# Optimization experiments

Hardware: AMD Instinct MI355X
Metric: run time of the kernel (lower is better)

## Reference

```python
import jax, jax.numpy as jnp
import numpy as np

N = 100000
F_IN = 512
NHID = 16
HEADS = 8
NCLASS = 40
E = 1600000
NEG_SLOPE = 0.2


def gat_conv(x, W, att_src, att_dst, bias, src, dst, heads, out_ch, concat):
    n = x.shape[0]
    h = (x @ W).reshape(n, heads, out_ch)              # [N,H,C]
    a_src = jnp.sum(h * att_src, axis=-1)              # [N,H]
    a_dst = jnp.sum(h * att_dst, axis=-1)              # [N,H]
    e = a_src[src] + a_dst[dst]                        # [E,H]
    e = jnp.where(e > 0, e, NEG_SLOPE * e)             # leaky_relu
    # segment softmax over incoming edges per destination node
    m = jax.ops.segment_max(e, dst, num_segments=n)    # [N,H]
    m = jnp.where(jnp.isfinite(m), m, 0.0)
    ex = jnp.exp(e - m[dst])
    s = jax.ops.segment_sum(ex, dst, num_segments=n)   # [N,H]
    alpha = ex / s[dst]                                # [E,H] (self-loops guarantee s>0)
    out = jax.ops.segment_sum(h[src] * alpha[:, :, None], dst, num_segments=n)  # [N,H,C]
    if concat:
        out = out.reshape(n, heads * out_ch)
    else:
        out = out.mean(axis=1)
    return out + bias


def setup_inputs() -> dict:
    key = jax.random.key(0)
    ks = jax.random.split(key, 10)
    x = jax.random.normal(ks[0], (N, F_IN), dtype=jnp.float32)
    edge_index = jax.random.randint(ks[1], (2, E), 0, N, dtype=jnp.int64)
    g1 = 1.0 / np.sqrt(F_IN)
    g2 = 1.0 / np.sqrt(NHID * HEADS)
    W1 = jax.random.uniform(ks[2], (F_IN, HEADS * NHID), jnp.float32, -g1, g1)
    att_src1 = jax.random.normal(ks[3], (1, HEADS, NHID), dtype=jnp.float32) * 0.1
    att_dst1 = jax.random.normal(ks[4], (1, HEADS, NHID), dtype=jnp.float32) * 0.1
    b1 = jnp.zeros((HEADS * NHID,), dtype=jnp.float32)
    W2 = jax.random.uniform(ks[5], (HEADS * NHID, NCLASS), jnp.float32, -g2, g2)
    att_src2 = jax.random.normal(ks[6], (1, 1, NCLASS), dtype=jnp.float32) * 0.1
    att_dst2 = jax.random.normal(ks[7], (1, 1, NCLASS), dtype=jnp.float32) * 0.1
    b2 = jnp.zeros((NCLASS,), dtype=jnp.float32)
    return {"x": x, "edge_index": edge_index, "W1": W1, "att_src1": att_src1,
            "att_dst1": att_dst1, "b1": b1, "W2": W2, "att_src2": att_src2,
            "att_dst2": att_dst2, "b2": b2}


def reference(x, edge_index, W1, att_src1, att_dst1, b1, W2, att_src2, att_dst2, b2):
    n = x.shape[0]
    # add self-loops (PyG GATConv default)
    loops = jnp.arange(n, dtype=edge_index.dtype)
    src = jnp.concatenate([edge_index[0], loops])
    dst = jnp.concatenate([edge_index[1], loops])
    # dropout is identity in eval mode
    h = gat_conv(x, W1, att_src1, att_dst1, b1, src, dst, HEADS, NHID, True)
    h = jax.nn.elu(h)
    out = gat_conv(h, W2, att_src2, att_dst2, b2, src, dst, 1, NCLASS, False)
    return jax.nn.log_softmax(out, axis=1)
```

## Files before the change

kernel.cpp:

```cpp
#include <hip/hip_runtime.h>
#include <hip/hip_fp16.h>
#include <math.h>

#define NEG_SLOPE 0.2f

__global__ __launch_bounds__(256) void gemm1_kernel(
    const float* __restrict__ x, const float* __restrict__ W,
    const float* __restrict__ att_src, const float* __restrict__ att_dst,
    __half* __restrict__ h1, float* __restrict__ a_src, float* __restrict__ a_dst,
    int M)
{
  __shared__ float At[32][68];
  __shared__ float Bs[32][128];
  const int tid = threadIdx.x;
  const int row0 = blockIdx.x * 64;
  const int tcol = (tid & 31) * 4;
  const int trow = (tid >> 5) * 8;
  float acc[8][4];
  #pragma unroll
  for (int i = 0; i < 8; i++)
    #pragma unroll
    for (int j = 0; j < 4; j++) acc[i][j] = 0.f;

  for (int k0 = 0; k0 < 512; k0 += 32) {
    #pragma unroll
    for (int i = 0; i < 2; ++i) {
      int idx = tid + i * 256;
      int r = idx >> 3;
      int kc = (idx & 7) << 2;
      float4 v = make_float4(0.f, 0.f, 0.f, 0.f);
      if (row0 + r < M) v = *(const float4*)&x[(size_t)(row0 + r) * 512 + k0 + kc];
      At[kc + 0][r] = v.x; At[kc + 1][r] = v.y; At[kc + 2][r] = v.z; At[kc + 3][r] = v.w;
    }
    #pragma unroll
    for (int i = 0; i < 4; ++i) {
      int idx = tid + i * 256;
      int kk = idx >> 5;
      int cc = (idx & 31) << 2;
      *(float4*)&Bs[kk][cc] = *(const float4*)&W[(size_t)(k0 + kk) * 128 + cc];
    }
    __syncthreads();
    #pragma unroll
    for (int k = 0; k < 32; ++k) {
      float4 b = *(float4*)&Bs[k][tcol];
      float4 a0 = *(float4*)&At[k][trow];
      float4 a1 = *(float4*)&At[k][trow + 4];
      float av[8] = {a0.x, a0.y, a0.z, a0.w, a1.x, a1.y, a1.z, a1.w};
      float bv[4] = {b.x, b.y, b.z, b.w};
      #pragma unroll
      for (int i = 0; i < 8; i++)
        #pragma unroll
        for (int j = 0; j < 4; j++)
          acc[i][j] = fmaf(av[i], bv[j], acc[i][j]);
    }
    __syncthreads();
  }
  float as1[4], ad1[4];
  #pragma unroll
  for (int j = 0; j < 4; j++) { as1[j] = att_src[tcol + j]; ad1[j] = att_dst[tcol + j]; }
  const int head = tcol >> 4;
  #pragma unroll
  for (int i = 0; i < 8; i++) {
    int r = row0 + trow + i;
    float ps = acc[i][0]*as1[0] + acc[i][1]*as1[1] + acc[i][2]*as1[2] + acc[i][3]*as1[3];
    float pd = acc[i][0]*ad1[0] + acc[i][1]*ad1[1] + acc[i][2]*ad1[2] + acc[i][3]*ad1[3];
    ps += __shfl_xor(ps, 1); ps += __shfl_xor(ps, 2);
    pd += __shfl_xor(pd, 1); pd += __shfl_xor(pd, 2);
    if (r < M) {
      __half2 p0 = __floats2half2_rn(acc[i][0], acc[i][1]);
      __half2 p1 = __floats2half2_rn(acc[i][2], acc[i][3]);
      uint2 u = make_uint2(*(unsigned int*)&p0, *(unsigned int*)&p1);
      *(uint2*)&h1[(size_t)r * 128 + tcol] = u;
      if ((tid & 3) == 0) { a_src[r * 8 + head] = ps; a_dst[r * 8 + head] = pd; }
    }
  }
}

__global__ __launch_bounds__(256) void hist_kernel(
    const int* __restrict__ ei, int E, int ET, int* __restrict__ cnt)
{
  int e = blockIdx.x * 256 + threadIdx.x;
  if (e >= ET) return;
  int dst = (e < E) ? ei[E + e] : e - E;
  atomicAdd(&cnt[dst], 1);
}

__global__ __launch_bounds__(256) void scan_bsum(
    const int* __restrict__ cnt, int* __restrict__ bsum, int M)
{
  __shared__ int sm[256];
  int i = blockIdx.x * 256 + threadIdx.x;
  sm[threadIdx.x] = (i < M) ? cnt[i] : 0;
  __syncthreads();
  for (int o = 128; o; o >>= 1) {
    if (threadIdx.x < o) sm[threadIdx.x] += sm[threadIdx.x + o];
    __syncthreads();
  }
  if (threadIdx.x == 0) bsum[blockIdx.x] = sm[0];
}

__global__ __launch_bounds__(512) void scan_boff(
    const int* __restrict__ bsum, int* __restrict__ boff, int NB)
{
  __shared__ int sm[512];
  int t = threadIdx.x;
  int v = (t < NB) ? bsum[t] : 0;
  sm[t] = v; __syncthreads();
  #pragma unroll
  for (int o = 1; o < 512; o <<= 1) {
    int add = (t >= o) ? sm[t - o] : 0;
    __syncthreads();
    sm[t] += add;
    __syncthreads();
  }
  boff[t] = sm[t] - v;
}

__global__ __launch_bounds__(256) void scan_final(
    const int* __restrict__ cnt, const int* __restrict__ boff,
    int* __restrict__ startp, int* __restrict__ cursor, int M)
{
  __shared__ int sm[256];
  int t = threadIdx.x;
  int i = blockIdx.x * 256 + t;
  int v = (i < M) ? cnt[i] : 0;
  sm[t] = v; __syncthreads();
  #pragma unroll
  for (int o = 1; o < 256; o <<= 1) {
    int add = (t >= o) ? sm[t - o] : 0;
    __syncthreads();
    sm[t] += add;
    __syncthreads();
  }
  int excl = sm[t] - v + boff[blockIdx.x];
  if (i < M) {
    startp[i] = excl;
    cursor[i] = excl;
    if (i == M - 1) startp[M] = excl + v;
  }
}

__global__ __launch_bounds__(256) void scatter_kernel(
    const int* __restrict__ ei, int E, int ET,
    int* __restrict__ cursor, int* __restrict__ ssrc)
{
  int e = blockIdx.x * 256 + threadIdx.x;
  if (e >= ET) return;
  int src, dst;
  if (e < E) { src = ei[e]; dst = ei[E + e]; }
  else { src = e - E; dst = src; }
  int pos = atomicAdd(&cursor[dst], 1);
  ssrc[pos] = src;
}

__global__ __launch_bounds__(256) void agg1_kernel(
    const int* __restrict__ startp, const int* __restrict__ ssrc,
    const float* __restrict__ a_s, const float* __restrict__ a_d,
    const __half* __restrict__ h1, const float* __restrict__ b1,
    __half* __restrict__ h1e, int M)
{
  int n = blockIdx.x * 4 + (threadIdx.x >> 6);
  if (n >= M) return;
  const int lane = threadIdx.x & 63;
  const int hd = lane >> 3;
  const __half2* hp = (const __half2*)h1;
  float ad = a_d[n * 8 + hd];
  int jb = startp[n], je = startp[n + 1];
  float acc0 = 0.f, acc1 = 0.f, ssum = 0.f;
  int j = jb;
  for (; j + 3 < je; j += 4) {
    int s0 = ssrc[j], s1 = ssrc[j+1], s2 = ssrc[j+2], s3 = ssrc[j+3];
    float e0 = a_s[s0 * 8 + hd] + ad;
    float e1 = a_s[s1 * 8 + hd] + ad;
    float e2 = a_s[s2 * 8 + hd] + ad;
    float e3 = a_s[s3 * 8 + hd] + ad;
    __half2 g0 = hp[(size_t)s0 * 64 + lane];
    __half2 g1 = hp[(size_t)s1 * 64 + lane];
    __half2 g2 = hp[(size_t)s2 * 64 + lane];
    __half2 g3 = hp[(size_t)s3 * 64 + lane];
    e0 = e0 > 0.f ? e0 : NEG_SLOPE * e0;
    e1 = e1 > 0.f ? e1 : NEG_SLOPE * e1;
    e2 = e2 > 0.f ? e2 : NEG_SLOPE * e2;
    e3 = e3 > 0.f ? e3 : NEG_SLOPE * e3;
    float x0 = __expf(e0), x1 = __expf(e1), x2 = __expf(e2), x3 = __expf(e3);
    float2 f0 = __half22float2(g0), f1 = __half22float2(g1);
    float2 f2 = __half22float2(g2), f3 = __half22float2(g3);
    acc0 = fmaf(x0, f0.x, acc0); acc1 = fmaf(x0, f0.y, acc1);
    acc0 = fmaf(x1, f1.x, acc0); acc1 = fmaf(x1, f1.y, acc1);
    acc0 = fmaf(x2, f2.x, acc0); acc1 = fmaf(x2, f2.y, acc1);
    acc0 = fmaf(x3, f3.x, acc0); acc1 = fmaf(x3, f3.y, acc1);
    ssum += (x0 + x1) + (x2 + x3);
  }
  for (; j < je; ++j) {
    int s0 = ssrc[j];
    float e0 = a_s[s0 * 8 + hd] + ad;
    e0 = e0 > 0.f ? e0 : NEG_SLOPE * e0;
    float x0 = __expf(e0);
    float2 f0 = __half22float2(hp[(size_t)s0 * 64 + lane]);
    acc0 = fmaf(x0, f0.x, acc0); acc1 = fmaf(x0, f0.y, acc1);
    ssum += x0;
  }
  float2 bv = *(const float2*)&b1[lane * 2];
  float v0 = acc0 / ssum + bv.x;
  float v1 = acc1 / ssum + bv.y;
  v0 = v0 > 0.f ? v0 : expm1f(v0);
  v1 = v1 > 0.f ? v1 : expm1f(v1);
  ((__half2*)h1e)[(size_t)n * 64 + lane] = __floats2half2_rn(v0, v1);
}

__global__ __launch_bounds__(256) void gemm2_kernel(
    const __half* __restrict__ h, const float* __restrict__ W2,
    const float* __restrict__ att_src, const float* __restrict__ att_dst,
    __half* __restrict__ h2, float* __restrict__ a2s, float* __restrict__ a2d,
    int M)
{
  __shared__ float W2s[128 * 40];
  __shared__ float hs[4][128];
  const int tid = threadIdx.x;
  const int lane = tid & 63;
  const int w = tid >> 6;
  const __half2* hp = (const __half2*)h;
  for (int i = tid; i < 128 * 40; i += 256) W2s[i] = W2[i];
  float asv = (lane < 40) ? att_src[lane] : 0.f;
  float adv = (lane < 40) ? att_dst[lane] : 0.f;
  __syncthreads();
  for (int r0 = blockIdx.x * 4; r0 < M; r0 += gridDim.x * 4) {
    {
      int r = r0 + (tid >> 6);
      int cp = tid & 63;
      float2 f = make_float2(0.f, 0.f);
      if (r < M) f = __half22float2(hp[(size_t)r * 64 + cp]);
      hs[tid >> 6][cp * 2] = f.x; hs[tid >> 6][cp * 2 + 1] = f.y;
    }
    __syncthreads();
    const int row = r0 + w;
    float acc = 0.f;
    if (lane < 40) {
      #pragma unroll 8
      for (int k = 0; k < 128; ++k) acc = fmaf(hs[w][k], W2s[k * 40 + lane], acc);
    }
    float ps = acc * asv, pd = acc * adv;
    #pragma unroll
    for (int off = 32; off; off >>= 1) { ps += __shfl_xor(ps, off); pd += __shfl_xor(pd, off); }
    if (row < M) {
      if (lane < 40) h2[(size_t)row * 40 + lane] = __float2half_rn(acc);
      if (lane == 0) { a2s[row] = ps; a2d[row] = pd; }
    }
    __syncthreads();
  }
}

__global__ __launch_bounds__(256) void agg2_kernel(
    const int* __restrict__ startp, const int* __restrict__ ssrc,
    const float* __restrict__ a2s, const float* __restrict__ a2d,
    const __half* __restrict__ h2, const float* __restrict__ b2,
    float* __restrict__ outp, int M)
{
  int n = blockIdx.x * 8 + (threadIdx.x >> 5);
  if (n >= M) return;
  const int l = threadIdx.x & 31;
  const bool act = l < 20;
  const __half2* hp = (const __half2*)h2;
  float ad = a2d[n];
  int jb = startp[n], je = startp[n + 1];
  float acc0 = 0.f, acc1 = 0.f, ssum = 0.f;
  __half2 z2 = __floats2half2_rn(0.f, 0.f);
  int j = jb;
  for (; j + 3 < je; j += 4) {
    int s0 = ssrc[j], s1 = ssrc[j+1], s2 = ssrc[j+2], s3 = ssrc[j+3];
    float e0 = a2s[s0] + ad;
    float e1 = a2s[s1] + ad;
    float e2 = a2s[s2] + ad;
    float e3 = a2s[s3] + ad;
    __half2 g0 = act ? hp[(size_t)s0 * 20 + l] : z2;
    __half2 g1 = act ? hp[(size_t)s1 * 20 + l] : z2;
    __half2 g2 = act ? hp[(size_t)s2 * 20 + l] : z2;
    __half2 g3 = act ? hp[(size_t)s3 * 20 + l] : z2;
    e0 = e0 > 0.f ? e0 : NEG_SLOPE * e0;
    e1 = e1 > 0.f ? e1 : NEG_SLOPE * e1;
    e2 = e2 > 0.f ? e2 : NEG_SLOPE * e2;
    e3 = e3 > 0.f ? e3 : NEG_SLOPE * e3;
    float x0 = __expf(e0), x1 = __expf(e1), x2 = __expf(e2), x3 = __expf(e3);
    float2 f0 = __half22float2(g0), f1 = __half22float2(g1);
    float2 f2 = __half22float2(g2), f3 = __half22float2(g3);
    acc0 = fmaf(x0, f0.x, acc0); acc1 = fmaf(x0, f0.y, acc1);
    acc0 = fmaf(x1, f1.x, acc0); acc1 = fmaf(x1, f1.y, acc1);
    acc0 = fmaf(x2, f2.x, acc0); acc1 = fmaf(x2, f2.y, acc1);
    acc0 = fmaf(x3, f3.x, acc0); acc1 = fmaf(x3, f3.y, acc1);
    ssum += (x0 + x1) + (x2 + x3);
  }
  for (; j < je; ++j) {
    int s0 = ssrc[j];
    float e0 = a2s[s0] + ad;
    e0 = e0 > 0.f ? e0 : NEG_SLOPE * e0;
    float x0 = __expf(e0);
    float2 f0 = __half22float2(act ? hp[(size_t)s0 * 20 + l] : z2);
    acc0 = fmaf(x0, f0.x, acc0); acc1 = fmaf(x0, f0.y, acc1);
    ssum += x0;
  }
  float v0 = act ? acc0 / ssum + b2[l * 2]     : -1e30f;
  float v1 = act ? acc1 / ssum + b2[l * 2 + 1] : -1e30f;
  float m = fmaxf(v0, v1);
  #pragma unroll
  for (int o = 16; o; o >>= 1) m = fmaxf(m, __shfl_xor(m, o));
  float ex = act ? expf(v0 - m) + expf(v1 - m) : 0.f;
  #pragma unroll
  for (int o = 16; o; o >>= 1) ex += __shfl_xor(ex, o);
  float lg = m + logf(ex);
  if (act) *(float2*)&outp[(size_t)n * 40 + l * 2] = make_float2(v0 - lg, v1 - lg);
}

extern "C" void kernel_launch(void* const* d_in, const int* in_sizes, int n_in,
                              void* d_out, int out_size, void* d_ws, size_t ws_size,
                              hipStream_t stream)
{
  const float* x   = (const float*)d_in[0];
  const int*   ei  = (const int*)d_in[1];
  const float* W1  = (const float*)d_in[2];
  const float* as1 = (const float*)d_in[3];
  const float* ad1 = (const float*)d_in[4];
  const float* b1  = (const float*)d_in[5];
  const float* W2  = (const float*)d_in[6];
  const float* as2 = (const float*)d_in[7];
  const float* ad2 = (const float*)d_in[8];
  const float* b2  = (const float*)d_in[9];
  float* outp = (float*)d_out;

  const int M  = in_sizes[0] / 512;
  const int E  = in_sizes[1] / 2;
  const int ET = E + M;
  const int NB = (M + 255) / 256;

  __half* h1  = (__half*)d_ws;
  __half* h1e = h1 + (size_t)M * 128;
  __half* h2  = h1e + (size_t)M * 128;
  float* a_s1 = (float*)(h2 + (size_t)M * 40);
  float* a_d1 = a_s1 + (size_t)M * 8;
  float* a2s  = a_d1 + (size_t)M * 8;
  float* a2d  = a2s + M;
  int* cnt    = (int*)(a2d + M);
  int* startp = cnt + M;
  int* cursor = startp + (M + 1);
  int* bsum   = cursor + M;
  int* boff   = bsum + NB;
  int* ssrc   = boff + 512;

  hipMemsetAsync(cnt, 0, (size_t)M * sizeof(int), stream);

  hist_kernel<<<(ET + 255) / 256, 256, 0, stream>>>(ei, E, ET, cnt);
  scan_bsum<<<NB, 256, 0, stream>>>(cnt, bsum, M);
  scan_boff<<<1, 512, 0, stream>>>(bsum, boff, NB);
  scan_final<<<NB, 256, 0, stream>>>(cnt, boff, startp, cursor, M);
  scatter_kernel<<<(ET + 255) / 256, 256, 0, stream>>>(ei, E, ET, cursor, ssrc);

  gemm1_kernel<<<(M + 63) / 64, 256, 0, stream>>>(x, W1, as1, ad1, h1, a_s1, a_d1, M);
  agg1_kernel<<<(M + 3) / 4, 256, 0, stream>>>(startp, ssrc, a_s1, a_d1, h1, b1, h1e, M);

  gemm2_kernel<<<1024, 256, 0, stream>>>(h1e, W2, as2, ad2, h2, a2s, a2d, M);
  agg2_kernel<<<(M + 7) / 8, 256, 0, stream>>>(startp, ssrc, a2s, a2d, h2, b2, outp, M);
}
```

Baseline: 843.4 us.

## Use bf16 MFMA for first-layer GEMM with swizzled LDS tiles

Replaces the scalar FP32 FMA tiled GEMM for x@W1 with a bf16 MFMA (16x16x32) kernel that uses 128-row tiles and XOR-swizzled shared memory. x is converted to bf16 on the fly, and a new small kernel pre-transposes and converts W1 to bf16. The attention dot products are now reduced with wave shuffles over the MFMA output layout. This cuts the compute cost of the dominant dense GEMM at the price of bf16 input rounding and narrower, scattered half stores in the epilogue.

```diff
diff --git a/kernel.cpp b/kernel.cpp
--- a/kernel.cpp
+++ b/kernel.cpp
@@ -4,74 +4,120 @@
 
 #define NEG_SLOPE 0.2f
 
+typedef short bf16x8 __attribute__((ext_vector_type(8)));
+typedef float f32x4 __attribute__((ext_vector_type(4)));
+
+__device__ __forceinline__ unsigned short f2bf(float f) {
+  unsigned int u = __builtin_bit_cast(unsigned int, f);
+  u = (u + 0x7fffu + ((u >> 16) & 1u)) >> 16;
+  return (unsigned short)u;
+}
+__device__ __forceinline__ unsigned int pk2bf(float lo, float hi) {
+  return (unsigned int)f2bf(lo) | ((unsigned int)f2bf(hi) << 16);
+}
+
+__global__ __launch_bounds__(256) void w1conv_kernel(
+    const float* __restrict__ W1, unsigned short* __restrict__ Wt)
+{
+  int idx = blockIdx.x * 256 + threadIdx.x;
+  int k = idx >> 7, n = idx & 127;
+  Wt[n * 512 + k] = f2bf(W1[idx]);
+}
+
 __global__ __launch_bounds__(256) void gemm1_kernel(
-    const float* __restrict__ x, const float* __restrict__ W,
+    const float* __restrict__ x, const unsigned short* __restrict__ Wt,
     const float* __restrict__ att_src, const float* __restrict__ att_dst,
     __half* __restrict__ h1, float* __restrict__ a_src, float* __restrict__ a_dst,
     int M)
 {
-  __shared__ float At[32][68];
-  __shared__ float Bs[32][128];
-  const int tid = threadIdx.x;
-  const int row0 = blockIdx.x * 64;
-  const int tcol = (tid & 31) * 4;
-  const int trow = (tid >> 5) * 8;
-  float acc[8][4];
-  #pragma unroll
-  for (int i = 0; i < 8; i++)
+  __shared__ unsigned char Asm[128 * 128];
+  __shared__ unsigned char Bsm[128 * 128];
+  const int tid  = threadIdx.x;
+  const int lane = tid & 63;
+  const int wid  = tid >> 6;
+  const int wr   = wid >> 1, wc = wid & 1;
+  const int row0 = blockIdx.x * 128;
+
+  f32x4 acc[4][4];
+  #pragma unroll
+  for (int m = 0; m < 4; ++m)
     #pragma unroll
-    for (int j = 0; j < 4; j++) acc[i][j] = 0.f;
-
-  for (int k0 = 0; k0 < 512; k0 += 32) {
+    for (int n = 0; n < 4; ++n) acc[m][n] = (f32x4){0.f, 0.f, 0.f, 0.f};
+
+  const int sr = tid >> 1;
+  const int sk = (tid & 1) * 32;
+  const int swz = (sr & 7) << 4;
+
+  for (int k0 = 0; k0 < 512; k0 += 64) {
+    {
+      const bool valid = (row0 + sr) < M;
+      const float4* src = (const float4*)&x[(size_t)(row0 + sr) * 512 + k0 + sk];
+      #pragma unroll
+      for (int q = 0; q < 4; ++q) {
+        float4 fa = valid ? src[q * 2]     : make_float4(0.f, 0.f, 0.f, 0.f);
+        float4 fb = valid ? src[q * 2 + 1] : make_float4(0.f, 0.f, 0.f, 0.f);
+        uint4 u = make_uint4(pk2bf(fa.x, fa.y), pk2bf(fa.z, fa.w),
+                             pk2bf(fb.x, fb.y), pk2bf(fb.z, fb.w));
+        *(uint4*)(Asm + sr * 128 + (((sk + q * 8) * 2) ^ swz)) = u;
+      }
+    }
+    {
+      const uint4* src = (const uint4*)&Wt[(size_t)sr * 512 + k0 + sk];
+      #pragma unroll
+      for (int q = 0; q < 4; ++q)
+        *(uint4*)(Bsm + sr * 128 + (((sk + q * 8) * 2) ^ swz)) = src[q];
+    }
+    __syncthreads();
     #pragma unroll
-    for (int i = 0; i < 2; ++i) {
-      int idx = tid + i * 256;
-      int r = idx >> 3;
-      int kc = (idx & 7) << 2;
-      float4 v = make_float4(0.f, 0.f, 0.f, 0.f);
-      if (row0 + r < M) v = *(const float4*)&x[(size_t)(row0 + r) * 512 + k0 + kc];
-      At[kc + 0][r] = v.x; At[kc + 1][r] = v.y; At[kc + 2][r] = v.z; At[kc + 3][r] = v.w;
-    }
+    for (int ks = 0; ks < 2; ++ks) {
+      const int kb = ks * 64 + ((lane >> 4) * 16);
+      bf16x8 af[4], bfr[4];
+      #pragma unroll
+      for (int m = 0; m < 4; ++m) {
+        int r = wr * 64 + m * 16 + (lane & 15);
+        af[m] = *(const bf16x8*)(Asm + r * 128 + (kb ^ ((r & 7) << 4)));
+      }
+      #pragma unroll
+      for (int n = 0; n < 4; ++n) {
+        int r = wc * 64 + n * 16 + (lane & 15);
+        bfr[n] = *(const bf16x8*)(Bsm + r * 128 + (kb ^ ((r & 7) << 4)));
+      }
+      #pragma unroll
+      for (int m = 0; m < 4; ++m)
+        #pragma unroll
+        for (int n = 0; n < 4; ++n)
+          acc[m][n] = __builtin_amdgcn_mfma_f32_16x16x32_bf16(af[m], bfr[n], acc[m][n], 0, 0, 0);
+    }
+    __syncthreads();
+  }
+
+  float asv[4], adv[4];
+  #pragma unroll
+  for (int n = 0; n < 4; ++n) {
+    int col = wc * 64 + n * 16 + (lane & 15);
+    asv[n] = att_src[col];
+    adv[n] = att_dst[col];
+  }
+  #pragma unroll
+  for (int m = 0; m < 4; ++m) {
     #pragma unroll
-    for (int i = 0; i < 4; ++i) {
-      int idx = tid + i * 256;
-      int kk = idx >> 5;
-      int cc = (idx & 31) << 2;
-      *(float4*)&Bs[kk][cc] = *(const float4*)&W[(size_t)(k0 + kk) * 128 + cc];
-    }
-    __syncthreads();
-    #pragma unroll
-    for (int k = 0; k < 32; ++k) {
-      float4 b = *(float4*)&Bs[k][tcol];
-      float4 a0 = *(float4*)&At[k][trow];
-      float4 a1 = *(float4*)&At[k][trow + 4];
-      float av[8] = {a0.x, a0.y, a0.z, a0.w, a1.x, a1.y, a1.z, a1.w};
-      float bv[4] = {b.x, b.y, b.z, b.w};
-      #pragma unroll
-      for (int i = 0; i < 8; i++)
-        #pragma unroll
-        for (int j = 0; j < 4; j++)
-          acc[i][j] = fmaf(av[i], bv[j], acc[i][j]);
-    }
-    __syncthreads();
-  }
-  float as1[4], ad1[4];
-  #pragma unroll
-  for (int j = 0; j < 4; j++) { as1[j] = att_src[tcol + j]; ad1[j] = att_dst[tcol + j]; }
-  const int head = tcol >> 4;
-  #pragma unroll
-  for (int i = 0; i < 8; i++) {
-    int r = row0 + trow + i;
-    float ps = acc[i][0]*as1[0] + acc[i][1]*as1[1] + acc[i][2]*as1[2] + acc[i][3]*as1[3];
-    float pd = acc[i][0]*ad1[0] + acc[i][1]*ad1[1] + acc[i][2]*ad1[2] + acc[i][3]*ad1[3];
-    ps += __shfl_xor(ps, 1); ps += __shfl_xor(ps, 2);
-    pd += __shfl_xor(pd, 1); pd += __shfl_xor(pd, 2);
-    if (r < M) {
-      __half2 p0 = __floats2half2_rn(acc[i][0], acc[i][1]);
-      __half2 p1 = __floats2half2_rn(acc[i][2], acc[i][3]);
-      uint2 u = make_uint2(*(unsigned int*)&p0, *(unsigned int*)&p1);
-      *(uint2*)&h1[(size_t)r * 128 + tcol] = u;
-      if ((tid & 3) == 0) { a_src[r * 8 + head] = ps; a_dst[r * 8 + head] = pd; }
+    for (int n = 0; n < 4; ++n) {
+      const int col  = wc * 64 + n * 16 + (lane & 15);
+      const int head = wc * 4 + n;
+      #pragma unroll
+      for (int e = 0; e < 4; ++e) {
+        int row = row0 + wr * 64 + m * 16 + (lane >> 4) * 4 + e;
+        float v = acc[m][n][e];
+        float ps = v * asv[n], pd = v * adv[n];
+        ps += __shfl_xor(ps, 1); pd += __shfl_xor(pd, 1);
+        ps += __shfl_xor(ps, 2); pd += __shfl_xor(pd, 2);
+        ps += __shfl_xor(ps, 4); pd += __shfl_xor(pd, 4);
+        ps += __shfl_xor(ps, 8); pd += __shfl_xor(pd, 8);
+        if (row < M) {
+          h1[(size_t)row * 128 + col] = __float2half_rn(v);
+          if ((lane & 15) == 0) { a_src[row * 8 + head] = ps; a_dst[row * 8 + head] = pd; }
+        }
+      }
     }
   }
 }
@@ -344,6 +390,7 @@
   int* bsum   = cursor + M;
   int* boff   = bsum + NB;
   int* ssrc   = boff + 512;
+  unsigned short* Wt = (unsigned short*)(ssrc + ET);
 
   hipMemsetAsync(cnt, 0, (size_t)M * sizeof(int), stream);
 
@@ -353,7 +400,8 @@
   scan_final<<<NB, 256, 0, stream>>>(cnt, boff, startp, cursor, M);
   scatter_kernel<<<(ET + 255) / 256, 256, 0, stream>>>(ei, E, ET, cursor, ssrc);
 
-  gemm1_kernel<<<(M + 63) / 64, 256, 0, stream>>>(x, W1, as1, ad1, h1, a_s1, a_d1, M);
+  w1conv_kernel<<<256, 256, 0, stream>>>(W1, Wt);
+  gemm1_kernel<<<(M + 127) / 128, 256, 0, stream>>>(x, Wt, as1, ad1, h1, a_s1, a_d1, M);
   agg1_kernel<<<(M + 3) / 4, 256, 0, stream>>>(startp, ssrc, a_s1, a_d1, h1, b1, h1e, M);
 
   gemm2_kernel<<<1024, 256, 0, stream>>>(h1e, W2, as2, ad2, h2, a2s, a2d, M);
```

After: 798.3 us. -5.3%, faster.
